# Optimization experiments

Measured on AMD Instinct MI355X. Metric: run time of the kernel, lower is better.

Reference implementation:

```python
import jax, jax.numpy as jnp
import numpy as np
import math

H = 8        # num_heads
DK = 64      # key_dim
DV = 64      # value_dim
FACTOR = 4


def setup_inputs() -> dict:
    key = jax.random.key(0)
    B, T, S, D = 4, 2048, 2048, 512
    Dout = H * DV
    ks = jax.random.split(key, 16)
    sample_k = min(int(FACTOR * math.log(S)), S)  # = 33
    inp = {
        "x_q": jax.random.normal(ks[0], (B, T, D), jnp.float32),
        "x_k": jax.random.normal(ks[1], (B, S, D), jnp.float32),
        "x_v": jax.random.normal(ks[2], (B, S, D), jnp.float32),
        "Wq": jax.random.normal(ks[3], (D, H * DK), jnp.float32) * 0.02,
        "bq": jnp.zeros((H * DK,), jnp.float32),
        "Wk": jax.random.normal(ks[4], (D, H * DK), jnp.float32) * 0.02,
        "bk": jnp.zeros((H * DK,), jnp.float32),
        "Wv": jax.random.normal(ks[5], (D, H * DV), jnp.float32) * 0.02,
        "bv": jnp.zeros((H * DV,), jnp.float32),
        "Wo": jax.random.normal(ks[6], (H * DV, Dout), jnp.float32) * 0.02,
        "bo": jnp.zeros((Dout,), jnp.float32),
        "index_sample": jax.random.randint(ks[7], (T, sample_k), 0, S, jnp.int32),
    }
    return inp


def reference(x_q, x_k, x_v, Wq, bq, Wk, bk, Wv, bv, Wo, bo, index_sample):
    B, T, D = x_q.shape
    S = x_k.shape[1]
    u = min(int(FACTOR * math.log(T)), T)  # n_top queries kept

    q = (x_q @ Wq + bq).reshape(B, T, H, DK)
    k = (x_k @ Wk + bk).reshape(B, S, H, DK)
    v = (x_v @ Wv + bv).reshape(B, S, H, DV)

    # --- _prob_QK: sampled QK to score queries ---
    ks = k[:, index_sample]                                  # [B,T,J,H,dk]
    qk_s = jnp.einsum('bthd,btjhd->bthj', q, ks)             # [B,T,H,J]
    M = qk_s.max(-1) - qk_s.mean(-1)                         # [B,T,H]
    _, top = jax.lax.top_k(jnp.transpose(M, (0, 2, 1)), u)   # [B,H,u]

    b_idx = jnp.arange(B)[:, None, None]
    h_idx = jnp.arange(H)[None, :, None]
    q_red = q[b_idx, top, h_idx]                             # [B,H,u,dk]
    qk = jnp.einsum('bhud,bshd->bhus', q_red, k)             # [B,H,u,S]

    # --- s0: default (no mask) context = mean of values over S ---
    ctx = jnp.broadcast_to(v.mean(axis=1, keepdims=True), (B, T, H, DV))
    ctx = jnp.transpose(ctx, (0, 2, 1, 3))                   # [B,H,T,dv]

    # --- s1: scaled softmax over full keys for top queries ---
    scores = jax.nn.softmax(qk * (1.0 / math.sqrt(DK)), axis=-1)
    attn = jnp.einsum('bhus,bshd->bhud', scores, v)          # [B,H,u,dv]

    # --- scatter top-query results into context / scores ---
    ctx = ctx.at[b_idx, h_idx, top].set(attn)                # [B,H,T,dv]
    final_scores = jnp.full((B, H, T, S), 1.0 / S, dtype=scores.dtype)
    final_scores = final_scores.at[b_idx, h_idx, top].set(scores)

    out = jnp.transpose(ctx, (0, 2, 1, 3)).reshape(B, T, H * DV)
    out = out @ Wo + bo                                      # [B,T,output_dim]
    return out, final_scores
```

## Files before the change

### kernel.cpp

```cpp
#include <hip/hip_runtime.h>

typedef __attribute__((ext_vector_type(8))) short short8;
typedef __attribute__((ext_vector_type(4))) float f32x4;

constexpr int Bn  = 4;
constexpr int Tn  = 2048;
constexpr int Sn  = 2048;
constexpr int Dn  = 512;
constexpr int Hn  = 8;
constexpr int DKn = 64;
constexpr int DVn = 64;
constexpr int HDn = 512;
constexpr int SKn = 30;
constexpr int Un  = 30;
constexpr int Gu  = 6;
constexpr int NGroups = Un / Gu;
constexpr int NAttnG  = Bn * Hn * NGroups;
constexpr int NOutF   = (Bn * Tn) / 8;
constexpr int NGemm  = 768;
constexpr float kScale = 0.125f;

constexpr int NWsplit = 192;
constexpr int NVPart  = 64;
constexpr int NSampled = Bn * Tn;

constexpr int NFillG = 7168;
constexpr int NFillS = 4608;
constexpr int NFillT = 4608;
constexpr int FillRowsG = 0;
constexpr int FillRowsS = NFillG * 4;
constexpr int FillRowsT = (NFillG + NFillS) * 4;

__device__ __forceinline__ ushort bf16_rne(float x) {
  unsigned u = __float_as_uint(x);
  return (ushort)((u + 0x7fffu + ((u >> 16) & 1u)) >> 16);
}
__device__ __forceinline__ float bf16f(ushort h) {
  return __uint_as_float(((unsigned)h) << 16);
}
__device__ __forceinline__ void nt_store4(f32x4* p, f32x4 v) {
  __builtin_nontemporal_store(v, p);
}
__device__ __forceinline__ void fill_rows4_256(float* fscores, size_t r0, int tid) {
  const float c = 1.0f / Sn;
  const f32x4 c4v = {c, c, c, c};
  f32x4* fs4 = (f32x4*)fscores + r0 * (Sn / 4);
#pragma unroll
  for (int i = 0; i < 8; ++i) nt_store4(fs4 + i * 256 + tid, c4v);
}
__device__ __forceinline__ void gload_lds16(const void* g, void* lds) {
  __builtin_amdgcn_global_load_lds((const __attribute__((address_space(1))) void*)g,
                                   (__attribute__((address_space(3))) void*)lds, 16, 0, 0);
}

#define MFMA(accv, av, bv) \
  asm volatile("v_mfma_f32_16x16x32_bf16 %0, %1, %2, %0" : "+v"(accv) : "v"(av), "v"(bv))

__global__ __launch_bounds__(256) void prep_split_kernel(
    const float* __restrict__ Wq, const float* __restrict__ Wk, const float* __restrict__ Wv,
    ushort* __restrict__ WtH, ushort* __restrict__ WtL) {
  const int tid = threadIdx.x;
  const int bid = blockIdx.x;

  const int z = bid / 64, t = bid % 64;
  const int k0 = (t >> 3) * 64, n0 = (t & 7) * 64;
  const float* W = (z == 0) ? Wq : (z == 1) ? Wk : Wv;
  __shared__ float tile[64][65];
  const int r = tid >> 2, c0 = (tid & 3) * 16;
#pragma unroll
  for (int i = 0; i < 16; i += 4) {
    const float4 vv = *(const float4*)(W + (size_t)(k0 + r) * HDn + n0 + c0 + i);
    tile[r][c0 + i] = vv.x; tile[r][c0 + i + 1] = vv.y;
    tile[r][c0 + i + 2] = vv.z; tile[r][c0 + i + 3] = vv.w;
  }
  __syncthreads();
  unsigned hp[8], lp[8];
#pragma unroll
  for (int i = 0; i < 16; i += 2) {
    const float x0 = tile[c0 + i][r];
    const float x1 = tile[c0 + i + 1][r];
    const ushort h0 = bf16_rne(x0), h1 = bf16_rne(x1);
    const ushort l0 = bf16_rne(x0 - bf16f(h0)), l1 = bf16_rne(x1 - bf16f(h1));
    hp[i >> 1] = (unsigned)h0 | ((unsigned)h1 << 16);
    lp[i >> 1] = (unsigned)l0 | ((unsigned)l1 << 16);
  }
  const size_t off = (size_t)(z * 512 + n0 + r) * 512 + k0 + c0;
  *(uint4*)(WtH + off)     = make_uint4(hp[0], hp[1], hp[2], hp[3]);
  *(uint4*)(WtH + off + 8) = make_uint4(hp[4], hp[5], hp[6], hp[7]);
  *(uint4*)(WtL + off)     = make_uint4(lp[0], lp[1], lp[2], lp[3]);
  *(uint4*)(WtL + off + 8) = make_uint4(lp[4], lp[5], lp[6], lp[7]);
}

__global__ __launch_bounds__(256, 2) void gemm_fill_kernel(
    const float* __restrict__ xq, const float* __restrict__ xk, const float* __restrict__ xv,
    const ushort* __restrict__ WtH, const ushort* __restrict__ WtL,
    const float* __restrict__ bq, const float* __restrict__ bk, const float* __restrict__ bv,
    float* __restrict__ qo, float* __restrict__ ko, float* __restrict__ vo,
    float* __restrict__ fscores) {
  const int bid = blockIdx.x;
  const int tid = threadIdx.x;

  if (bid >= NGemm) {
    fill_rows4_256(fscores, (size_t)FillRowsG + (size_t)(bid - NGemm) * 4, tid);
    return;
  }

  __shared__ ushort AsH[64][32];
  __shared__ ushort AsL[64][32];
  __shared__ ushort BsH[256][32];
  __shared__ ushort BsL[256][32];

  const int z = bid >> 8;
  const int rem = bid & 255;
  const int bm = (rem >> 1) * 64;
  const int bn = (rem & 1) * 256;
  const float* X = (z == 0) ? xq : (z == 1) ? xk : xv;
  const float* bias = (z == 0) ? bq : (z == 1) ? bk : bv;
  float* Y = (z == 0) ? qo : (z == 1) ? ko : vo;

  const int lane = tid & 63;
  const int wave = tid >> 6;
  const int fr = lane & 15;
  const int gk = lane >> 4;

  const int ar = tid >> 2, ag = tid & 3;
  const float* xrow = X + (size_t)(bm + ar) * Dn + ag * 8;
  const int agq = (ag ^ ((ar >> 1) & 3)) * 8;

  const int gsrc = (lane & 3) ^ ((lane >> 3) & 3);
  const ushort* bgH = WtH + (size_t)(z * 512 + bn + wave * 64 + (lane >> 2)) * 512 + gsrc * 8;
  const ushort* bgL = WtL + (size_t)(z * 512 + bn + wave * 64 + (lane >> 2)) * 512 + gsrc * 8;
  ushort* ldsH0 = &BsH[wave * 64][0];
  ushort* ldsL0 = &BsL[wave * 64][0];

  const int gq = (gk ^ ((fr >> 1) & 3)) * 8;

  f32x4 acc[4][4];
#pragma unroll
  for (int m = 0; m < 4; ++m)
#pragma unroll
    for (int n = 0; n < 4; ++n)
#pragma unroll
      for (int j = 0; j < 4; ++j) acc[m][n][j] = 0.f;

  float4 af0 = *(const float4*)(xrow + 0);
  float4 af1 = *(const float4*)(xrow + 4);

  for (int k0 = 0; k0 < Dn; k0 += 32) {
    __syncthreads();
#pragma unroll
    for (int c = 0; c < 4; ++c) {
      gload_lds16(bgH + k0 + c * 8192, ldsH0 + c * 512);
      gload_lds16(bgL + k0 + c * 8192, ldsL0 + c * 512);
    }
    {
      float xf[8] = {af0.x, af0.y, af0.z, af0.w, af1.x, af1.y, af1.z, af1.w};
      unsigned hp[4], lp[4];
#pragma unroll
      for (int i = 0; i < 8; i += 2) {
        const ushort h0 = bf16_rne(xf[i]), h1 = bf16_rne(xf[i + 1]);
        const ushort l0 = bf16_rne(xf[i] - bf16f(h0)), l1 = bf16_rne(xf[i + 1] - bf16f(h1));
        hp[i >> 1] = (unsigned)h0 | ((unsigned)h1 << 16);
        lp[i >> 1] = (unsigned)l0 | ((unsigned)l1 << 16);
      }
      *(uint4*)&AsH[ar][agq] = make_uint4(hp[0], hp[1], hp[2], hp[3]);
      *(uint4*)&AsL[ar][agq] = make_uint4(lp[0], lp[1], lp[2], lp[3]);
    }
    if (k0 + 32 < Dn) {
      af0 = *(const float4*)(xrow + k0 + 32);
      af1 = *(const float4*)(xrow + k0 + 36);
    }
    __syncthreads();

    short8 aH[4], aL[4], bH[4], bL[4];
#pragma unroll
    for (int m = 0; m < 4; ++m) {
      aH[m] = *(const short8*)&AsH[m * 16 + fr][gq];
      aL[m] = *(const short8*)&AsL[m * 16 + fr][gq];
    }
#pragma unroll
    for (int n = 0; n < 4; ++n) {
      bH[n] = *(const short8*)&BsH[wave * 64 + n * 16 + fr][gq];
      bL[n] = *(const short8*)&BsL[wave * 64 + n * 16 + fr][gq];
    }
#pragma unroll
    for (int m = 0; m < 4; ++m)
#pragma unroll
      for (int n = 0; n < 4; ++n) {
        MFMA(acc[m][n], aH[m], bH[n]);
        MFMA(acc[m][n], aH[m], bL[n]);
        MFMA(acc[m][n], aL[m], bH[n]);
      }
  }
  asm volatile("s_nop 7\n\ts_nop 7");

  float bsv[4];
#pragma unroll
  for (int n = 0; n < 4; ++n) bsv[n] = bias[bn + wave * 64 + n * 16 + fr];
#pragma unroll
  for (int m = 0; m < 4; ++m) {
#pragma unroll
    for (int n = 0; n < 4; ++n) {
      const int col = bn + wave * 64 + n * 16 + fr;
#pragma unroll
      for (int j = 0; j < 4; ++j) {
        Y[(size_t)(bm + m * 16 + gk * 4 + j) * HDn + col] = acc[m][n][j] + bsv[n];
      }
    }
  }
}

__global__ __launch_bounds__(64) void sampled_m_kernel(
    const float* __restrict__ q, const float* __restrict__ k,
    const int* __restrict__ idxs, float* __restrict__ Mt,
    const float* __restrict__ v, float* __restrict__ vpart,
    float* __restrict__ fscores) {
  const int bid = blockIdx.x;
  const int lane = threadIdx.x;

  if (bid >= NVPart + NSampled) {
    const size_t r0 = (size_t)FillRowsS + (size_t)(bid - NVPart - NSampled) * 4;
    const float c = 1.0f / Sn;
    const f32x4 c4v = {c, c, c, c};
    f32x4* p = (f32x4*)fscores + r0 * (Sn / 4);
#pragma unroll
    for (int i = 0; i < 32; ++i) nt_store4(p + i * 64 + lane, c4v);
    return;
  }

  if (bid < NVPart) {
    const int pb = bid;
    const int b = pb >> 4, part = pb & 15;
    const float4* v4 = (const float4*)(v + (size_t)b * Sn * HDn);
    float4 a0 = make_float4(0.f, 0.f, 0.f, 0.f);
    float4 a1 = make_float4(0.f, 0.f, 0.f, 0.f);
    const int s0 = part * 128;
    for (int s = s0; s < s0 + 128; ++s) {
      const float4 x0 = v4[(size_t)s * 128 + lane * 2];
      const float4 x1 = v4[(size_t)s * 128 + lane * 2 + 1];
      a0.x += x0.x; a0.y += x0.y; a0.z += x0.z; a0.w += x0.w;
      a1.x += x1.x; a1.y += x1.y; a1.z += x1.z; a1.w += x1.w;
    }
    float4* vp4 = (float4*)vpart + (size_t)pb * 128;
    vp4[lane * 2] = a0; vp4[lane * 2 + 1] = a1;
    return;
  }

  const int inner = bid - NVPart;
  const int b = inner >> 11, t = inner & (Tn - 1);

  const int sg = lane >> 3;
  const int d8 = lane & 7;
  __shared__ int sidx[32];
  if (lane < SKn) sidx[lane] = idxs[t * SKn + lane];
  if (lane >= SKn && lane < 32) sidx[lane] = 0;
  __syncthreads();
  const float* qrow = q + ((size_t)(b * Tn + t)) * HDn;
  const float* kb = k + (size_t)b * Sn * HDn;
  for (int h = 0; h < Hn; ++h) {
    const float4 qv0 = *(const float4*)(qrow + h * DKn + d8 * 8);
    const float4 qv1 = *(const float4*)(qrow + h * DKn + d8 * 8 + 4);
    float mx = -1e30f, sum = 0.f;
#pragma unroll
    for (int jb = 0; jb < 32; jb += 8) {
      const int j = jb + sg;
      const int srow = sidx[j];
      const float* kr = kb + (size_t)srow * HDn + h * DKn + d8 * 8;
      const float4 kv0 = *(const float4*)kr;
      const float4 kv1 = *(const float4*)(kr + 4);
      float p = kv0.x * qv0.x + kv0.y * qv0.y + kv0.z * qv0.z + kv0.w * qv0.w
              + kv1.x * qv1.x + kv1.y * qv1.y + kv1.z * qv1.z + kv1.w * qv1.w;
      p += __shfl_xor(p, 1);
      p += __shfl_xor(p, 2);
      p += __shfl_xor(p, 4);
      if (j < SKn) { mx = fmaxf(mx, p); sum += p; }
    }
    mx = fmaxf(mx, __shfl_xor(mx, 8));
    mx = fmaxf(mx, __shfl_xor(mx, 16));
    mx = fmaxf(mx, __shfl_xor(mx, 32));
    sum += __shfl_xor(sum, 8);
    sum += __shfl_xor(sum, 16);
    sum += __shfl_xor(sum, 32);
    if (lane == 0) Mt[((size_t)(b * Hn + h)) * Tn + t] = mx - sum * (1.0f / SKn);
  }
}

__global__ __launch_bounds__(256) void topk_vmean_base_kernel(
    const float* __restrict__ Mt, const float* __restrict__ vpart,
    const float* __restrict__ Wo, const float* __restrict__ bo,
    int* __restrict__ top, float* __restrict__ vmean, float* __restrict__ basep,
    float* __restrict__ fscores) {
  const int tid = threadIdx.x;
  const int lane = tid & 63, w = tid >> 6;

  if (blockIdx.x >= 36) {
    fill_rows4_256(fscores, (size_t)FillRowsT + (size_t)(blockIdx.x - 36) * 4, tid);
    return;
  }

  __shared__ float vals[Tn];
  __shared__ float wv[4];
  __shared__ int wi[4];
  __shared__ float4 part[256];
  __shared__ float vm[HDn];

  if (blockIdx.x < 32) {
    const int bh = blockIdx.x;
    for (int i = tid; i < Tn; i += 256) vals[i] = Mt[(size_t)bh * Tn + i];
    __syncthreads();
    for (int u = 0; u < Un; ++u) {
      float bv = -1e30f; int bi = 0x7fffffff;
      for (int i = tid; i < Tn; i += 256) {
        const float x = vals[i];
        if (x > bv) { bv = x; bi = i; }
      }
#pragma unroll
      for (int o = 1; o < 64; o <<= 1) {
        const float ov = __shfl_xor(bv, o);
        const int oi = __shfl_xor(bi, o);
        if (ov > bv || (ov == bv && oi < bi)) { bv = ov; bi = oi; }
      }
      if (lane == 0) { wv[w] = bv; wi[w] = bi; }
      __syncthreads();
      bv = wv[0]; bi = wi[0];
#pragma unroll
      for (int j = 1; j < 4; ++j) {
        if (wv[j] > bv || (wv[j] == bv && wi[j] < bi)) { bv = wv[j]; bi = wi[j]; }
      }
      if (tid == 0) { top[bh * Un + u] = bi; vals[bi] = -1e30f; }
      __syncthreads();
    }
  } else {
    const int b = blockIdx.x - 32;
    const int c4 = tid & 127, half = tid >> 7;
    float4 acc = make_float4(0.f, 0.f, 0.f, 0.f);
    for (int p = half * 8; p < half * 8 + 8; ++p) {
      const float4 x = ((const float4*)vpart)[(size_t)(b * 16 + p) * 128 + c4];
      acc.x += x.x; acc.y += x.y; acc.z += x.z; acc.w += x.w;
    }
    part[tid] = acc;
    __syncthreads();
    if (half == 0) {
      float4 a = part[c4], bpp = part[128 + c4];
      const float sc = 1.0f / Sn;
      float4 r = make_float4((a.x + bpp.x) * sc, (a.y + bpp.y) * sc,
                             (a.z + bpp.z) * sc, (a.w + bpp.w) * sc);
      *(float4*)(vm + c4 * 4) = r;
      *(float4*)(vmean + b * HDn + c4 * 4) = r;
    }
    __syncthreads();
    const float4* Wo4 = (const float4*)Wo;
    float4 acc2 = make_float4(0.f, 0.f, 0.f, 0.f);
    for (int c = half * 256; c < half * 256 + 256; ++c) {
      const float vmc = vm[c];
      const float4 wrow = Wo4[(size_t)c * 128 + c4];
      acc2.x += vmc * wrow.x; acc2.y += vmc * wrow.y;
      acc2.z += vmc * wrow.z; acc2.w += vmc * wrow.w;
    }
    __syncthreads();
    part[tid] = acc2;
    __syncthreads();
    if (half == 0) {
      float4 a = part[c4], bpp = part[128 + c4];
      const float4 bb = ((const float4*)bo)[c4];
      float4 r = make_float4(a.x + bpp.x + bb.x, a.y + bpp.y + bb.y,
                             a.z + bpp.z + bb.z, a.w + bpp.w + bb.w);
      ((float4*)basep)[b * 128 + c4] = r;
    }
  }
}

__global__ __launch_bounds__(256) void attn_out_kernel(
    const float* __restrict__ q, const float* __restrict__ k,
    const float* __restrict__ v, const float* __restrict__ vmean,
    const int* __restrict__ top, const float* __restrict__ Wo,
    const float* __restrict__ basep,
    float* __restrict__ out, float* __restrict__ fscores) {
  const int tid = threadIdx.x;
  const int bid = blockIdx.x;

  if (bid >= NAttnG) {
    const int fid = bid - NAttnG;
    const int r0 = fid * 8;
    const int b = r0 >> 11;
    const int t0 = r0 & (Tn - 1);
    __shared__ int sflag8[8];
    if (tid < 8) sflag8[tid] = 0;
    __syncthreads();
    if (tid < Hn * Un) {
      const int d = top[b * Hn * Un + tid] - t0;
      if (d >= 0 && d < 8) sflag8[d] = 1;
    }
    __syncthreads();
    const int col4 = tid & 127, rh = tid >> 7;
    const float4 bv4 = ((const float4*)basep)[b * 128 + col4];
    const f32x4 bvx = {bv4.x, bv4.y, bv4.z, bv4.w};
#pragma unroll
    for (int rp = 0; rp < 4; ++rp) {
      const int rr = rp * 2 + rh;
      float4* orow4 = (float4*)(out + (size_t)(r0 + rr) * HDn) + col4;
      if (sflag8[rr]) {
        float* p = (float*)orow4;
        atomicAdd(p + 0, bv4.x); atomicAdd(p + 1, bv4.y);
        atomicAdd(p + 2, bv4.z); atomicAdd(p + 3, bv4.w);
      } else {
        nt_store4((f32x4*)orow4, bvx);
      }
    }
    return;
  }

  const int xs = bid & 7;
  const int b = xs & 3;
  const int combo = (bid >> 3) + (xs >> 2) * 20;
  const int h = combo / 5;
  const int grp = combo % 5;
  const int bh = b * Hn + h;
  const int u0 = grp * Gu;
  const int lane = tid & 63, w = tid >> 6;

  __shared__ float qs[Gu][DKn];
  __shared__ float sc[Gu][2052];
  __shared__ float red[8];
  __shared__ int tsel[Gu];
  __shared__ float4 partv[4][Gu][16];

  if (tid < Gu) tsel[tid] = top[bh * Un + u0 + tid];
  __syncthreads();
  for (int i = tid; i < Gu * DKn; i += 256) {
    const int g = i >> 6, d = i & 63;
    qs[g][d] = q[((size_t)(b * Tn + tsel[g])) * HDn + h * DKn + d];
  }
  __syncthreads();

  const float4* k4 = (const float4*)k;
  for (int s = tid; s < Sn; s += 256) {
    const float4* krow = k4 + ((size_t)(b * Sn + s)) * 128 + h * 16;
    float acc[Gu];
#pragma unroll
    for (int g = 0; g < Gu; ++g) acc[g] = 0.f;
#pragma unroll
    for (int d4i = 0; d4i < 16; ++d4i) {
      const float4 kv = krow[d4i];
#pragma unroll
      for (int g = 0; g < Gu; ++g) {
        const float4 qv = *(const float4*)&qs[g][d4i * 4];
        acc[g] += kv.x * qv.x + kv.y * qv.y + kv.z * qv.z + kv.w * qv.w;
      }
    }
#pragma unroll
    for (int g = 0; g < Gu; ++g) sc[g][s] = acc[g] * kScale;
  }
  __syncthreads();

  float invs[Gu];
#pragma unroll
  for (int g = 0; g < Gu; ++g) {
    float lm = -1e30f;
    for (int i = tid; i < Sn; i += 256) lm = fmaxf(lm, sc[g][i]);
#pragma unroll
    for (int o = 1; o < 64; o <<= 1) lm = fmaxf(lm, __shfl_xor(lm, o));
    if (lane == 0) red[w] = lm;
    __syncthreads();
    const float mx = fmaxf(fmaxf(red[0], red[1]), fmaxf(red[2], red[3]));
    float ls = 0.f;
    for (int i = tid; i < Sn; i += 256) {
      const float e = __expf(sc[g][i] - mx);
      sc[g][i] = e;
      ls += e;
    }
#pragma unroll
    for (int o = 1; o < 64; o <<= 1) ls += __shfl_xor(ls, o);
    if (lane == 0) red[4 + w] = ls;
    __syncthreads();
    invs[g] = 1.0f / (red[4] + red[5] + red[6] + red[7]);
    __syncthreads();
  }
#pragma unroll
  for (int g = 0; g < Gu; ++g) {
    const float inv = invs[g];
    float4* scg4 = (float4*)sc[g];
    f32x4* fsrow4 = (f32x4*)(fscores + ((size_t)bh * Tn + tsel[g]) * Sn);
#pragma unroll
    for (int it = 0; it < 2; ++it) {
      const int i = it * 256 + tid;
      float4 p = scg4[i];
      p.x *= inv; p.y *= inv; p.z *= inv; p.w *= inv;
      scg4[i] = p;
      const f32x4 px = {p.x, p.y, p.z, p.w};
      nt_store4(fsrow4 + i, px);
    }
  }
  __syncthreads();

  const int d4 = lane & 15;
  const int sg = (w << 2) + (lane >> 4);
  const float4* v4 = (const float4*)v;
  float4 pacc[Gu];
#pragma unroll
  for (int g = 0; g < Gu; ++g) pacc[g] = make_float4(0.f, 0.f, 0.f, 0.f);
  for (int s = sg; s < Sn; s += 16) {
    const float4 vv = v4[((size_t)(b * Sn + s)) * 128 + h * 16 + d4];
#pragma unroll
    for (int g = 0; g < Gu; ++g) {
      const float p = sc[g][s];
      pacc[g].x += p * vv.x; pacc[g].y += p * vv.y;
      pacc[g].z += p * vv.z; pacc[g].w += p * vv.w;
    }
  }
#pragma unroll
  for (int g = 0; g < Gu; ++g) {
#pragma unroll
    for (int o = 16; o < 64; o <<= 1) {
      pacc[g].x += __shfl_xor(pacc[g].x, o);
      pacc[g].y += __shfl_xor(pacc[g].y, o);
      pacc[g].z += __shfl_xor(pacc[g].z, o);
      pacc[g].w += __shfl_xor(pacc[g].w, o);
    }
    if (lane < 16) partv[w][g][lane] = pacc[g];
  }
  __syncthreads();
  if (tid < Gu * 16) {
    const int g = tid >> 4, dd = tid & 15;
    float4 r = partv[0][g][dd];
    const float4 r1 = partv[1][g][dd], r2 = partv[2][g][dd], r3 = partv[3][g][dd];
    r.x += r1.x + r2.x + r3.x; r.y += r1.y + r2.y + r3.y;
    r.z += r1.z + r2.z + r3.z; r.w += r1.w + r2.w + r3.w;
    const float4 vm4 = ((const float4*)vmean)[bh * 16 + dd];
    r.x -= vm4.x; r.y -= vm4.y; r.z -= vm4.z; r.w -= vm4.w;
    *(float4*)&qs[g][dd * 4] = r;
  }
  __syncthreads();

  const int col4 = tid & 127, gg = tid >> 7;
  const float4* Wo4 = (const float4*)Wo;
#pragma unroll
  for (int gp = 0; gp < Gu / 2; ++gp) {
    const int g = gp * 2 + gg;
    float4 a = make_float4(0.f, 0.f, 0.f, 0.f);
#pragma unroll
    for (int d = 0; d < DKn; ++d) {
      const float dv = qs[g][d];
      const float4 wrow = Wo4[(size_t)(h * DKn + d) * 128 + col4];
      a.x += dv * wrow.x; a.y += dv * wrow.y;
      a.z += dv * wrow.z; a.w += dv * wrow.w;
    }
    float* orow = out + ((size_t)(b * Tn + tsel[g])) * HDn + col4 * 4;
    atomicAdd(orow + 0, a.x); atomicAdd(orow + 1, a.y);
    atomicAdd(orow + 2, a.z); atomicAdd(orow + 3, a.w);
  }
}

extern "C" void kernel_launch(void* const* d_in, const int* in_sizes, int n_in,
                              void* d_out, int out_size, void* d_ws, size_t ws_size,
                              hipStream_t stream) {
  const float* x_q = (const float*)d_in[0];
  const float* x_k = (const float*)d_in[1];
  const float* x_v = (const float*)d_in[2];
  const float* Wq = (const float*)d_in[3];
  const float* bq = (const float*)d_in[4];
  const float* Wk = (const float*)d_in[5];
  const float* bk = (const float*)d_in[6];
  const float* Wv = (const float*)d_in[7];
  const float* bv = (const float*)d_in[8];
  const float* Wo = (const float*)d_in[9];
  const float* bo = (const float*)d_in[10];
  const int* idx = (const int*)d_in[11];

  float* out = (float*)d_out;
  float* fscores = out + (size_t)Bn * Tn * HDn;

  float* ws = (float*)d_ws;
  float* q = ws;
  float* kp = ws + (size_t)4194304;
  float* vp = ws + (size_t)8388608;
  float* Mt = ws + (size_t)12582912;
  float* vmean = ws + (size_t)12648448;
  float* basep = ws + (size_t)12650496;
  int* top = (int*)(ws + (size_t)12652544);
  float* vpart = ws + (size_t)12656640;

  char* scr = (char*)(fscores + (size_t)49152 * Sn);
  ushort* WtH = (ushort*)scr;
  ushort* WtL = WtH + (size_t)3 * 512 * 512;

  prep_split_kernel<<<NWsplit, 256, 0, stream>>>(Wq, Wk, Wv, WtH, WtL);

  gemm_fill_kernel<<<NGemm + NFillG, 256, 0, stream>>>(
      x_q, x_k, x_v, WtH, WtL, bq, bk, bv, q, kp, vp, fscores);

  sampled_m_kernel<<<NVPart + NSampled + NFillS, 64, 0, stream>>>(
      q, kp, idx, Mt, vp, vpart, fscores);

  topk_vmean_base_kernel<<<36 + NFillT, 256, 0, stream>>>(
      Mt, vpart, Wo, bo, top, vmean, basep, fscores);

  attn_out_kernel<<<NAttnG + NOutF, 256, 0, stream>>>(
      q, kp, vp, vmean, top, Wo, basep, out, fscores);
}
```

Before: 765.5 us.

## Map all heads across wavefront lanes in sampled QK scoring, rebalance fill blocks

```diff
diff --git a/kernel.cpp b/kernel.cpp
--- a/kernel.cpp
+++ b/kernel.cpp
@@ -24,9 +24,9 @@
 constexpr int NVPart  = 64;
 constexpr int NSampled = Bn * Tn;
 
-constexpr int NFillG = 7168;
-constexpr int NFillS = 4608;
-constexpr int NFillT = 4608;
+constexpr int NFillG = 9216;
+constexpr int NFillS = 2048;
+constexpr int NFillT = 5120;
 constexpr int FillRowsG = 0;
 constexpr int FillRowsS = NFillG * 4;
 constexpr int FillRowsT = (NFillG + NFillS) * 4;
@@ -249,39 +249,32 @@
   const int inner = bid - NVPart;
   const int b = inner >> 11, t = inner & (Tn - 1);
 
-  const int sg = lane >> 3;
-  const int d8 = lane & 7;
   __shared__ int sidx[32];
   if (lane < SKn) sidx[lane] = idxs[t * SKn + lane];
-  if (lane >= SKn && lane < 32) sidx[lane] = 0;
-  __syncthreads();
-  const float* qrow = q + ((size_t)(b * Tn + t)) * HDn;
-  const float* kb = k + (size_t)b * Sn * HDn;
-  for (int h = 0; h < Hn; ++h) {
-    const float4 qv0 = *(const float4*)(qrow + h * DKn + d8 * 8);
-    const float4 qv1 = *(const float4*)(qrow + h * DKn + d8 * 8 + 4);
-    float mx = -1e30f, sum = 0.f;
-#pragma unroll
-    for (int jb = 0; jb < 32; jb += 8) {
-      const int j = jb + sg;
-      const int srow = sidx[j];
-      const float* kr = kb + (size_t)srow * HDn + h * DKn + d8 * 8;
-      const float4 kv0 = *(const float4*)kr;
-      const float4 kv1 = *(const float4*)(kr + 4);
-      float p = kv0.x * qv0.x + kv0.y * qv0.y + kv0.z * qv0.z + kv0.w * qv0.w
-              + kv1.x * qv1.x + kv1.y * qv1.y + kv1.z * qv1.z + kv1.w * qv1.w;
-      p += __shfl_xor(p, 1);
-      p += __shfl_xor(p, 2);
-      p += __shfl_xor(p, 4);
-      if (j < SKn) { mx = fmaxf(mx, p); sum += p; }
-    }
-    mx = fmaxf(mx, __shfl_xor(mx, 8));
-    mx = fmaxf(mx, __shfl_xor(mx, 16));
-    mx = fmaxf(mx, __shfl_xor(mx, 32));
-    sum += __shfl_xor(sum, 8);
-    sum += __shfl_xor(sum, 16);
-    sum += __shfl_xor(sum, 32);
-    if (lane == 0) Mt[((size_t)(b * Hn + h)) * Tn + t] = mx - sum * (1.0f / SKn);
+  __syncthreads();
+
+  const float* qrow = q + ((size_t)(b * Tn + t)) * HDn + lane * 8;
+  const float4 qv0 = *(const float4*)qrow;
+  const float4 qv1 = *(const float4*)(qrow + 4);
+  const float* kb = k + (size_t)b * Sn * HDn + lane * 8;
+
+  float mx = -1e30f, sum = 0.f;
+#pragma unroll 5
+  for (int j = 0; j < SKn; ++j) {
+    const float* kr = kb + (size_t)sidx[j] * HDn;
+    const float4 kv0 = *(const float4*)kr;
+    const float4 kv1 = *(const float4*)(kr + 4);
+    float p = kv0.x * qv0.x + kv0.y * qv0.y + kv0.z * qv0.z + kv0.w * qv0.w
+            + kv1.x * qv1.x + kv1.y * qv1.y + kv1.z * qv1.z + kv1.w * qv1.w;
+    p += __shfl_xor(p, 1);
+    p += __shfl_xor(p, 2);
+    p += __shfl_xor(p, 4);
+    mx = fmaxf(mx, p);
+    sum += p;
+  }
+  if ((lane & 7) == 0) {
+    const int h = lane >> 3;
+    Mt[((size_t)(b * Hn + h)) * Tn + t] = mx - sum * (1.0f / SKn);
   }
 }
 
```

New measurement: 770.9 us. About the same (+0.7%).
